# Performance work log

Measured on AMD Instinct MI355X. Metric: run time of the kernel, lower is better.

The kernel has to match this reference:

```python
import jax, jax.numpy as jnp
import numpy as np
from jax import lax

INPUT_DIM = 16
H1 = 5
H2 = 50
NUM_CLASSES = 20
B = 4096
T = 512


def _lstm(x, w_ih, w_hh, b_ih, b_hh, hidden):
    # x: [B, T, D]; PyTorch LSTM gate order i, f, g, o; returns all hidden states [B, T, H]
    xg = jnp.einsum('btd,gd->btg', x, w_ih) + (b_ih + b_hh)  # [B, T, 4H]
    xg_t = jnp.swapaxes(xg, 0, 1)  # [T, B, 4H]
    h0 = jnp.zeros((x.shape[0], hidden), x.dtype)
    c0 = jnp.zeros((x.shape[0], hidden), x.dtype)

    def step(carry, xt):
        h, c = carry
        g = xt + h @ w_hh.T  # [B, 4H]
        i, f, gg, o = jnp.split(g, 4, axis=-1)
        i = jax.nn.sigmoid(i)
        f = jax.nn.sigmoid(f)
        gg = jnp.tanh(gg)
        o = jax.nn.sigmoid(o)
        c = f * c + i * gg
        h = o * jnp.tanh(c)
        return (h, c), h

    _, hs = lax.scan(step, (h0, c0), xg_t)
    return jnp.swapaxes(hs, 0, 1)  # [B, T, H]


def setup_inputs() -> dict:
    key = jax.random.key(0)
    ks = jax.random.split(key, 12)
    s1 = 1.0 / np.sqrt(H1)
    s2 = 1.0 / np.sqrt(H2)
    u = lambda k, shape, s: jax.random.uniform(k, shape, jnp.float32, -s, s)
    return {
        'x': jax.random.normal(ks[0], (B, T, INPUT_DIM), jnp.float32),
        'w_ih1': u(ks[1], (4 * H1, INPUT_DIM), s1),
        'w_hh1': u(ks[2], (4 * H1, H1), s1),
        'b_ih1': u(ks[3], (4 * H1,), s1),
        'b_hh1': u(ks[4], (4 * H1,), s1),
        'w_ih2': u(ks[5], (4 * H2, H1), s2),
        'w_hh2': u(ks[6], (4 * H2, H2), s2),
        'b_ih2': u(ks[7], (4 * H2,), s2),
        'b_hh2': u(ks[8], (4 * H2,), s2),
        'fc_w': u(ks[9], (NUM_CLASSES, H2), s2),
        'fc_b': u(ks[10], (NUM_CLASSES,), s2),
    }


def reference(x, w_ih1, w_hh1, b_ih1, b_hh1, w_ih2, w_hh2, b_ih2, b_hh2, fc_w, fc_b):
    h1 = _lstm(x, w_ih1, w_hh1, b_ih1, b_hh1, H1)   # [B, T, 5]
    h2 = _lstm(h1, w_ih2, w_hh2, b_ih2, b_hh2, H2)  # [B, T, 50]
    feat = h2[:, -1, :]  # last timestep; dropout is identity in eval mode
    out = feat @ fc_w.T + fc_b  # [B, num_classes]
    return (out, feat)
```

## Files before the change

kernel.cpp:

```cpp
#include <hip/hip_runtime.h>
#include <stdint.h>

#define B_TOTAL 4096
#define T_STEPS 512
#define IN_DIM 16
#define H1 5
#define H2 50
#define NCLS 20
#define XFS 40

typedef __attribute__((ext_vector_type(8))) short bf16x8;
typedef __attribute__((ext_vector_type(4))) float f32x4;

#define LOG2E 1.44269504f
#define C2L   2.88539008f
#define C2L2  5.77078016f

__device__ inline float rcp1pexp2(float y){
  return __builtin_amdgcn_rcpf(1.0f + __builtin_amdgcn_exp2f(y));
}

__device__ inline unsigned pack_top(float a, float b){
  return __builtin_amdgcn_perm(__float_as_uint(a), __float_as_uint(b), 0x07060302u);
}
__device__ inline void cvt_store(unsigned short* dh, unsigned short* dl, float4 v){
  uint2 H, L;
  H.x = pack_top(v.y, v.x);
  H.y = pack_top(v.w, v.z);
  float r0 = v.x - __uint_as_float(__float_as_uint(v.x) & 0xFFFF0000u);
  float r1 = v.y - __uint_as_float(__float_as_uint(v.y) & 0xFFFF0000u);
  float r2 = v.z - __uint_as_float(__float_as_uint(v.z) & 0xFFFF0000u);
  float r3 = v.w - __uint_as_float(__float_as_uint(v.w) & 0xFFFF0000u);
  L.x = pack_top(r1, r0);
  L.y = pack_top(r3, r2);
  *(uint2*)dh = H; *(uint2*)dl = L;
}
__device__ inline void split1(float h, unsigned short& hi, unsigned short& lo){
  unsigned u = __float_as_uint(h);
  hi = (unsigned short)(u >> 16);
  float r = h - __uint_as_float(u & 0xFFFF0000u);
  lo = (unsigned short)(__float_as_uint(r) >> 16);
}
__device__ inline void wsplit(float w, short& hi, short& lo){
  unsigned u = __float_as_uint(w);
  hi = (short)(u >> 16);
  float r = w - __uint_as_float(u & 0xFFFF0000u);
  lo = (short)(__float_as_uint(r) >> 16);
}
__device__ inline void xsplit(float4 a, float4 b, bf16x8& H, bf16x8& L){
  short h,l;
  wsplit(a.x,h,l); H[0]=h; L[0]=l;
  wsplit(a.y,h,l); H[1]=h; L[1]=l;
  wsplit(a.z,h,l); H[2]=h; L[2]=l;
  wsplit(a.w,h,l); H[3]=h; L[3]=l;
  wsplit(b.x,h,l); H[4]=h; L[4]=l;
  wsplit(b.y,h,l); H[5]=h; L[5]=l;
  wsplit(b.z,h,l); H[6]=h; L[6]=l;
  wsplit(b.w,h,l); H[7]=h; L[7]=l;
}

#define LDS_FENCE() __asm__ volatile("s_waitcnt lgkmcnt(0)" ::: "memory")
#define BARRIER()   __asm__ volatile("s_barrier" ::: "memory")

__global__ __launch_bounds__(256, 1) void lstm_fused_kernel(
    const float* __restrict__ x,
    const float* __restrict__ w_ih1, const float* __restrict__ w_hh1,
    const float* __restrict__ b_ih1, const float* __restrict__ b_hh1,
    const float* __restrict__ w_ih2, const float* __restrict__ w_hh2,
    const float* __restrict__ b_ih2, const float* __restrict__ b_hh2,
    const float* __restrict__ fc_w, const float* __restrict__ fc_b,
    float* __restrict__ out)
{
  const int tid  = threadIdx.x;
  const int lane = tid & 63;
  const int wave = tid >> 6;
  const int l15  = lane & 15;
  const int quad = lane >> 4;
  const int b0   = blockIdx.x * 16;

  __shared__ __align__(16) unsigned short a2h[2][16*72], a2l[2][16*72];
  __shared__ __align__(16) unsigned short xfh[2][16*XFS], xfl[2][16*XFS];
  __shared__ float h2f[16*52];

  const bf16x8 zero8 = {0,0,0,0,0,0,0,0};
  const f32x4  zero4 = {0.f,0.f,0.f,0.f};

  bf16x8 Bh[4][3], Bl[4][3];
  f32x4 biasv[4];
  float cst[4] = {0.f,0.f,0.f,0.f};

  const int rsw = ((l15 >> 3) & 1) << 3;
  const int wsw = (quad >> 1) << 3;

#pragma unroll
  for (int tt=0; tt<4; ++tt)
#pragma unroll
    for (int kt=0; kt<3; ++kt){ Bh[tt][kt]=zero8; Bl[tt][kt]=zero8; }

  if (wave < 3){
    const int c = wave*16 + l15;
#pragma unroll
    for (int tt=0; tt<4; ++tt){
      const float gsc = (tt == 2) ? C2L : LOG2E;
      const int grow = tt*H2 + c;
#pragma unroll
      for (int kt=0; kt<2; ++kt){
#pragma unroll
        for (int j=0;j<8;j++){
          const int kk = kt*32 + quad*8 + j;
          float w = 0.f;
          if (kk < H2)         w = w_hh2[grow*H2 + kk];
          else if (kk < H2+H1) w = w_ih2[grow*H1 + (kk-H2)];
          w *= gsc;
          short hi, lo; wsplit(w, hi, lo);
          Bh[tt][kt][j] = hi; Bl[tt][kt][j] = lo;
        }
      }
      const float bias = gsc * (b_ih2[grow] + b_hh2[grow]);
      biasv[tt][0]=bias; biasv[tt][1]=bias; biasv[tt][2]=bias; biasv[tt][3]=bias;
    }
  } else {
#pragma unroll
    for (int tt=0; tt<4; ++tt){
      const float gsc = (tt == 2) ? C2L : LOG2E;
      float bias = 0.f;
      if (l15 < 2){
        const int grow = tt*H2 + 48 + l15;
#pragma unroll
        for (int kt=0; kt<2; ++kt){
#pragma unroll
          for (int j=0;j<8;j++){
            const int kk = kt*32 + quad*8 + j;
            float w = 0.f;
            if (kk < H2)         w = w_hh2[grow*H2 + kk];
            else if (kk < H2+H1) w = w_ih2[grow*H1 + (kk-H2)];
            w *= gsc;
            short hi, lo; wsplit(w, hi, lo);
            Bh[tt][kt][j] = hi; Bl[tt][kt][j] = lo;
          }
        }
        bias = gsc * (b_ih2[grow] + b_hh2[grow]);
      } else if (l15 < 7){
        const int e = l15 - 2;
        const int grow = tt*H1 + e;
#pragma unroll
        for (int j=0;j<8;j++){
          const int kk = 32 + quad*8 + j;
          float w1 = (kk >= H2 && kk < H2+H1) ? gsc * w_hh1[grow*H1 + (kk-H2)] : 0.f;
          short hi, lo; wsplit(w1, hi, lo);
          Bh[tt][1][j] = hi; Bl[tt][1][j] = lo;
          const int k2 = quad*8 + j;
          float w2 = (k2 < IN_DIM) ? gsc * w_ih1[grow*IN_DIM + k2] : 0.f;
          wsplit(w2, hi, lo);
          Bh[tt][2][j] = hi; Bl[tt][2][j] = lo;
        }
        bias = gsc * (b_ih1[grow] + b_hh1[grow]);
      }
      biasv[tt][0]=bias; biasv[tt][1]=bias; biasv[tt][2]=bias; biasv[tt][3]=bias;
    }
  }

  { unsigned short* p = &a2h[0][0]; for (int i=tid;i<2*16*72;i+=256)  p[i]=0; }
  { unsigned short* p = &a2l[0][0]; for (int i=tid;i<2*16*72;i+=256)  p[i]=0; }
  { unsigned short* p = &xfh[0][0]; for (int i=tid;i<2*16*XFS;i+=256) p[i]=0; }
  { unsigned short* p = &xfl[0][0]; for (int i=tid;i<2*16*XFS;i+=256) p[i]=0; }
  __syncthreads();

  const bool xprod = (wave == 0);
  const int pxb = lane >> 2;
  const int pxd = (lane & 3) * 4;
  const float* pxbase = &x[(size_t)(b0+pxb)*T_STEPS*IN_DIM + pxd];
  float4 PA, PB;
  if (xprod){
    float4 v1 = *(const float4*)(pxbase + 1*IN_DIM);
    cvt_store(&xfh[1][pxb*XFS+pxd], &xfl[1][pxb*XFS+pxd], v1);
    PA = *(const float4*)(pxbase + 2*IN_DIM);
  }

  if (wave == 3){
    bf16x8 XAh = zero8, XAl = zero8;
    if (quad < 2){
      const float* xp = &x[(size_t)(b0+l15)*T_STEPS*IN_DIM + quad*8];
      xsplit(*(const float4*)xp, *(const float4*)(xp+4), XAh, XAl);
    }
    f32x4 acc[4];
#pragma unroll
    for (int tt=0; tt<4; ++tt){
      f32x4 c2 = __builtin_amdgcn_mfma_f32_16x16x32_bf16(XAh, Bh[tt][2], biasv[tt], 0,0,0);
      c2 = __builtin_amdgcn_mfma_f32_16x16x32_bf16(XAl, Bh[tt][2], c2, 0,0,0);
      c2 = __builtin_amdgcn_mfma_f32_16x16x32_bf16(XAh, Bl[tt][2], c2, 0,0,0);
      acc[tt] = c2;
    }
    const bool isl1 = (l15 >= 2) && (l15 < 7);
#pragma unroll
    for (int r=0;r<4;r++){
      float gi = rcp1pexp2(-acc[0][r]);
      float gf = rcp1pexp2(-acc[1][r]);
      float gg = fmaf(-C2L2, rcp1pexp2(acc[2][r]), C2L);
      float go = rcp1pexp2(-acc[3][r]);
      float cn = fmaf(gf, cst[r], gi * gg);
      if (isl1){
        cst[r] = cn;
        float h = go * fmaf(-2.0f, rcp1pexp2(cn), 1.0f);
        unsigned short hh, hl; split1(h, hh, hl);
        const int row = quad*4 + r;
        a2h[0][row*72 + ((48 + l15) ^ wsw)] = hh;
        a2l[0][row*72 + ((48 + l15) ^ wsw)] = hl;
      }
    }
  }
  LDS_FENCE(); BARRIER();

#define MAIN_BODY(T_, RD_, WR_, PXW_, PXL_, LAST_) do { \
    if (xprod){ \
      cvt_store(&xfh[RD_][pxb*XFS+pxd], &xfl[RD_][pxb*XFS+pxd], PXW_);  \
      const int nidx_ = ((T_)+3 < T_STEPS) ? (T_)+3 : T_STEPS-1; \
      PXL_ = *(const float4*)(pxbase + (size_t)nidx_*IN_DIM);           \
    } \
    const int rb_ = l15*72; \
    bf16x8 ah0 = *(const bf16x8*)&a2h[RD_][rb_ +      ((quad*8) ^ rsw)]; \
    bf16x8 al0 = *(const bf16x8*)&a2l[RD_][rb_ +      ((quad*8) ^ rsw)]; \
    bf16x8 ah1 = *(const bf16x8*)&a2h[RD_][rb_ + 32 + ((quad*8) ^ rsw)]; \
    bf16x8 al1 = *(const bf16x8*)&a2l[RD_][rb_ + 32 + ((quad*8) ^ rsw)]; \
    f32x4 acc[4]; \
    if (wave < 3){ \
      _Pragma("unroll") \
      for (int tt=0; tt<4; ++tt){ \
        f32x4 c0 = __builtin_amdgcn_mfma_f32_16x16x32_bf16(ah0, Bh[tt][0], biasv[tt], 0,0,0); \
        c0 = __builtin_amdgcn_mfma_f32_16x16x32_bf16(al0, Bh[tt][0], c0, 0,0,0); \
        c0 = __builtin_amdgcn_mfma_f32_16x16x32_bf16(ah0, Bl[tt][0], c0, 0,0,0); \
        f32x4 c1 = __builtin_amdgcn_mfma_f32_16x16x32_bf16(ah1, Bh[tt][1], zero4, 0,0,0); \
        c1 = __builtin_amdgcn_mfma_f32_16x16x32_bf16(al1, Bh[tt][1], c1, 0,0,0); \
        c1 = __builtin_amdgcn_mfma_f32_16x16x32_bf16(ah1, Bl[tt][1], c1, 0,0,0); \
        acc[tt] = c0 + c1; \
      } \
    } else { \
      bf16x8 xfH = *(const bf16x8*)&xfh[WR_][l15*XFS + quad*8]; \
      bf16x8 xfL = *(const bf16x8*)&xfl[WR_][l15*XFS + quad*8]; \
      _Pragma("unroll") \
      for (int tt=0; tt<4; ++tt){ \
        f32x4 c0 = __builtin_amdgcn_mfma_f32_16x16x32_bf16(ah0, Bh[tt][0], biasv[tt], 0,0,0); \
        c0 = __builtin_amdgcn_mfma_f32_16x16x32_bf16(al0, Bh[tt][0], c0, 0,0,0); \
        c0 = __builtin_amdgcn_mfma_f32_16x16x32_bf16(ah0, Bl[tt][0], c0, 0,0,0); \
        f32x4 c1 = __builtin_amdgcn_mfma_f32_16x16x32_bf16(ah1, Bh[tt][1], zero4, 0,0,0); \
        c1 = __builtin_amdgcn_mfma_f32_16x16x32_bf16(al1, Bh[tt][1], c1, 0,0,0); \
        c1 = __builtin_amdgcn_mfma_f32_16x16x32_bf16(ah1, Bl[tt][1], c1, 0,0,0); \
        f32x4 c2 = __builtin_amdgcn_mfma_f32_16x16x32_bf16(xfH, Bh[tt][2], zero4, 0,0,0); \
        c2 = __builtin_amdgcn_mfma_f32_16x16x32_bf16(xfL, Bh[tt][2], c2, 0,0,0); \
        c2 = __builtin_amdgcn_mfma_f32_16x16x32_bf16(xfH, Bl[tt][2], c2, 0,0,0); \
        acc[tt] = (c0 + c1) + c2; \
      } \
    } \
     \
    if (wave < 3){ \
      const int wrb = quad*4*72 + ((wave*16 + l15) ^ wsw); \
      _Pragma("unroll") \
      for (int r=0;r<4;r++){ \
        float gi = rcp1pexp2(-acc[0][r]); \
        float gf = rcp1pexp2(-acc[1][r]); \
        float gg = fmaf(-C2L2, rcp1pexp2(acc[2][r]), C2L); \
        float go = rcp1pexp2(-acc[3][r]); \
        cst[r] = fmaf(gf, cst[r], gi * gg); \
        float h = go * fmaf(-2.0f, rcp1pexp2(cst[r]), 1.0f); \
        unsigned short hh, hl; split1(h, hh, hl); \
        a2h[WR_][wrb + r*72] = hh; \
        a2l[WR_][wrb + r*72] = hl; \
        if (LAST_){ \
          out[(size_t)B_TOTAL*NCLS + (size_t)(b0+quad*4+r)*H2 + wave*16+l15] = h; \
          h2f[(quad*4+r)*52 + wave*16+l15] = h; \
        } \
      } \
    } else { \
      const int wrb = quad*4*72 + ((48 + l15) ^ wsw);   \
      const bool wv_ = l15 < 7; \
      _Pragma("unroll") \
      for (int r=0;r<4;r++){ \
        float gi = rcp1pexp2(-acc[0][r]); \
        float gf = rcp1pexp2(-acc[1][r]); \
        float gg = fmaf(-C2L2, rcp1pexp2(acc[2][r]), C2L); \
        float go = rcp1pexp2(-acc[3][r]); \
        cst[r] = fmaf(gf, cst[r], gi * gg); \
        float h = go * fmaf(-2.0f, rcp1pexp2(cst[r]), 1.0f); \
        if (wv_){ \
          unsigned short hh, hl; split1(h, hh, hl); \
          a2h[WR_][wrb + r*72] = hh; \
          a2l[WR_][wrb + r*72] = hl; \
          if (LAST_ && l15 < 2){ \
            out[(size_t)B_TOTAL*NCLS + (size_t)(b0+quad*4+r)*H2 + 48+l15] = h; \
            h2f[(quad*4+r)*52 + 48+l15] = h; \
          } \
        } \
      } \
    } \
  } while(0)

  for (int t2 = 0; t2 < T_STEPS-2; t2 += 2){
    MAIN_BODY(t2,   0, 1, PA, PB, 0);
    LDS_FENCE(); BARRIER();
    MAIN_BODY(t2+1, 1, 0, PB, PA, 0);
    LDS_FENCE(); BARRIER();
  }
  MAIN_BODY(T_STEPS-2, 0, 1, PA, PB, 0);
  LDS_FENCE(); BARRIER();
  MAIN_BODY(T_STEPS-1, 1, 0, PB, PA, 1);

#undef MAIN_BODY

  __syncthreads();
  for (int i = tid; i < 16*NCLS; i += 256){
    const int b = i / NCLS, o = i % NCLS;
    float s = fc_b[o];
#pragma unroll 10
    for (int k=0;k<H2;k++) s += fc_w[o*H2+k] * h2f[b*52+k];
    out[(size_t)(b0+b)*NCLS + o] = s;
  }
}

extern "C" void kernel_launch(void* const* d_in, const int* in_sizes, int n_in,
                              void* d_out, int out_size, void* d_ws, size_t ws_size,
                              hipStream_t stream) {
  const float* x     = (const float*)d_in[0];
  const float* w_ih1 = (const float*)d_in[1];
  const float* w_hh1 = (const float*)d_in[2];
  const float* b_ih1 = (const float*)d_in[3];
  const float* b_hh1 = (const float*)d_in[4];
  const float* w_ih2 = (const float*)d_in[5];
  const float* w_hh2 = (const float*)d_in[6];
  const float* b_ih2 = (const float*)d_in[7];
  const float* b_hh2 = (const float*)d_in[8];
  const float* fc_w  = (const float*)d_in[9];
  const float* fc_b  = (const float*)d_in[10];
  float* out = (float*)d_out;

  lstm_fused_kernel<<<dim3(B_TOTAL/16), dim3(256), 0, stream>>>(
      x, w_ih1, w_hh1, b_ih1, b_hh1, w_ih2, w_hh2, b_ih2, b_hh2, fc_w, fc_b, out);
}
```

Measured before the change: 592.8 us.

## Process two 16-row batch groups per block to interleave independent recurrences

Each block now handles 32 batch rows as two independent 16-row groups, with separate cell state, x prefetch and LDS buffers. Both groups' MFMA chains and activations are interleaved within each timestep, so the latency of one group can overlap with work on the other. The cost is half as many blocks, which leaves half the CUs idle on a 256-CU part, and more register and LDS use per block.

```diff
diff --git a/kernel.cpp b/kernel.cpp
--- a/kernel.cpp
+++ b/kernel.cpp
@@ -76,18 +76,19 @@
   const int wave = tid >> 6;
   const int l15  = lane & 15;
   const int quad = lane >> 4;
-  const int b0   = blockIdx.x * 16;
-
-  __shared__ __align__(16) unsigned short a2h[2][16*72], a2l[2][16*72];
-  __shared__ __align__(16) unsigned short xfh[2][16*XFS], xfl[2][16*XFS];
-  __shared__ float h2f[16*52];
+  const int b0   = blockIdx.x * 32;
+
+  __shared__ __align__(16) unsigned short a2h[2][32*72], a2l[2][32*72];
+  __shared__ __align__(16) unsigned short xfh[2][32*XFS], xfl[2][32*XFS];
+  __shared__ float h2f[32*52];
 
   const bf16x8 zero8 = {0,0,0,0,0,0,0,0};
   const f32x4  zero4 = {0.f,0.f,0.f,0.f};
 
   bf16x8 Bh[4][3], Bl[4][3];
   f32x4 biasv[4];
-  float cst[4] = {0.f,0.f,0.f,0.f};
+  float cstA[4] = {0.f,0.f,0.f,0.f};
+  float cstB[4] = {0.f,0.f,0.f,0.f};
 
   const int rsw = ((l15 >> 3) & 1) << 3;
   const int wsw = (quad >> 1) << 3;
@@ -160,69 +161,113 @@
     }
   }
 
-  { unsigned short* p = &a2h[0][0]; for (int i=tid;i<2*16*72;i+=256)  p[i]=0; }
-  { unsigned short* p = &a2l[0][0]; for (int i=tid;i<2*16*72;i+=256)  p[i]=0; }
-  { unsigned short* p = &xfh[0][0]; for (int i=tid;i<2*16*XFS;i+=256) p[i]=0; }
-  { unsigned short* p = &xfl[0][0]; for (int i=tid;i<2*16*XFS;i+=256) p[i]=0; }
+  { unsigned short* p = &a2h[0][0]; for (int i=tid;i<2*32*72;i+=256)  p[i]=0; }
+  { unsigned short* p = &a2l[0][0]; for (int i=tid;i<2*32*72;i+=256)  p[i]=0; }
+  { unsigned short* p = &xfh[0][0]; for (int i=tid;i<2*32*XFS;i+=256) p[i]=0; }
+  { unsigned short* p = &xfl[0][0]; for (int i=tid;i<2*32*XFS;i+=256) p[i]=0; }
   __syncthreads();
 
   const bool xprod = (wave == 0);
   const int pxb = lane >> 2;
   const int pxd = (lane & 3) * 4;
-  const float* pxbase = &x[(size_t)(b0+pxb)*T_STEPS*IN_DIM + pxd];
-  float4 PA, PB;
+  const float* pxbaseA = &x[(size_t)(b0+pxb   )*T_STEPS*IN_DIM + pxd];
+  const float* pxbaseB = &x[(size_t)(b0+16+pxb)*T_STEPS*IN_DIM + pxd];
+  float4 PA_A, PA_B, PB_A, PB_B;
   if (xprod){
-    float4 v1 = *(const float4*)(pxbase + 1*IN_DIM);
-    cvt_store(&xfh[1][pxb*XFS+pxd], &xfl[1][pxb*XFS+pxd], v1);
-    PA = *(const float4*)(pxbase + 2*IN_DIM);
+    float4 v1a = *(const float4*)(pxbaseA + 1*IN_DIM);
+    float4 v1b = *(const float4*)(pxbaseB + 1*IN_DIM);
+    cvt_store(&xfh[1][pxb*XFS+pxd],      &xfl[1][pxb*XFS+pxd],      v1a);
+    cvt_store(&xfh[1][(16+pxb)*XFS+pxd], &xfl[1][(16+pxb)*XFS+pxd], v1b);
+    PA_A = *(const float4*)(pxbaseA + 2*IN_DIM);
+    PA_B = *(const float4*)(pxbaseB + 2*IN_DIM);
   }
 
   if (wave == 3){
-    bf16x8 XAh = zero8, XAl = zero8;
-    if (quad < 2){
-      const float* xp = &x[(size_t)(b0+l15)*T_STEPS*IN_DIM + quad*8];
-      xsplit(*(const float4*)xp, *(const float4*)(xp+4), XAh, XAl);
+#pragma unroll
+    for (int g=0; g<2; ++g){
+      bf16x8 XAh = zero8, XAl = zero8;
+      if (quad < 2){
+        const float* xp = &x[(size_t)(b0+g*16+l15)*T_STEPS*IN_DIM + quad*8];
+        xsplit(*(const float4*)xp, *(const float4*)(xp+4), XAh, XAl);
+      }
+      f32x4 acc[4];
+#pragma unroll
+      for (int tt=0; tt<4; ++tt){
+        f32x4 c2 = __builtin_amdgcn_mfma_f32_16x16x32_bf16(XAh, Bh[tt][2], biasv[tt], 0,0,0);
+        c2 = __builtin_amdgcn_mfma_f32_16x16x32_bf16(XAl, Bh[tt][2], c2, 0,0,0);
+        c2 = __builtin_amdgcn_mfma_f32_16x16x32_bf16(XAh, Bl[tt][2], c2, 0,0,0);
+        acc[tt] = c2;
+      }
+      const bool isl1 = (l15 >= 2) && (l15 < 7);
+#pragma unroll
+      for (int r=0;r<4;r++){
+        float gi = rcp1pexp2(-acc[0][r]);
+        float gf = rcp1pexp2(-acc[1][r]);
+        float gg = fmaf(-C2L2, rcp1pexp2(acc[2][r]), C2L);
+        float go = rcp1pexp2(-acc[3][r]);
+        float cn0 = (g==0) ? cstA[r] : cstB[r];
+        float cn = fmaf(gf, cn0, gi * gg);
+        if (isl1){
+          if (g==0) cstA[r] = cn; else cstB[r] = cn;
+          float h = go * fmaf(-2.0f, rcp1pexp2(cn), 1.0f);
+          unsigned short hh, hl; split1(h, hh, hl);
+          const int row = g*16 + quad*4 + r;
+          a2h[0][row*72 + ((48 + l15) ^ wsw)] = hh;
+          a2l[0][row*72 + ((48 + l15) ^ wsw)] = hl;
+        }
+      }
     }
-    f32x4 acc[4];
-#pragma unroll
-    for (int tt=0; tt<4; ++tt){
-      f32x4 c2 = __builtin_amdgcn_mfma_f32_16x16x32_bf16(XAh, Bh[tt][2], biasv[tt], 0,0,0);
-      c2 = __builtin_amdgcn_mfma_f32_16x16x32_bf16(XAl, Bh[tt][2], c2, 0,0,0);
-      c2 = __builtin_amdgcn_mfma_f32_16x16x32_bf16(XAh, Bl[tt][2], c2, 0,0,0);
-      acc[tt] = c2;
-    }
-    const bool isl1 = (l15 >= 2) && (l15 < 7);
-#pragma unroll
-    for (int r=0;r<4;r++){
-      float gi = rcp1pexp2(-acc[0][r]);
-      float gf = rcp1pexp2(-acc[1][r]);
-      float gg = fmaf(-C2L2, rcp1pexp2(acc[2][r]), C2L);
-      float go = rcp1pexp2(-acc[3][r]);
-      float cn = fmaf(gf, cst[r], gi * gg);
-      if (isl1){
-        cst[r] = cn;
-        float h = go * fmaf(-2.0f, rcp1pexp2(cn), 1.0f);
-        unsigned short hh, hl; split1(h, hh, hl);
-        const int row = quad*4 + r;
-        a2h[0][row*72 + ((48 + l15) ^ wsw)] = hh;
-        a2l[0][row*72 + ((48 + l15) ^ wsw)] = hl;
-      }
-    }
   }
   LDS_FENCE(); BARRIER();
 
-#define MAIN_BODY(T_, RD_, WR_, PXW_, PXL_, LAST_) do { \
-    if (xprod){ \
-      cvt_store(&xfh[RD_][pxb*XFS+pxd], &xfl[RD_][pxb*XFS+pxd], PXW_);  \
-      const int nidx_ = ((T_)+3 < T_STEPS) ? (T_)+3 : T_STEPS-1; \
-      PXL_ = *(const float4*)(pxbase + (size_t)nidx_*IN_DIM);           \
+#define ACT_STORE(ACC_, CST_, GO_, WR_, LAST_) do { \
+    if (wave < 3){ \
+      const int wrb = ((GO_) + quad*4)*72 + ((wave*16 + l15) ^ wsw); \
+      _Pragma("unroll") \
+      for (int r=0;r<4;r++){ \
+        float gi = rcp1pexp2(-ACC_[0][r]); \
+        float gf = rcp1pexp2(-ACC_[1][r]); \
+        float gg = fmaf(-C2L2, rcp1pexp2(ACC_[2][r]), C2L); \
+        float go = rcp1pexp2(-ACC_[3][r]); \
+        CST_[r] = fmaf(gf, CST_[r], gi * gg); \
+        float h = go * fmaf(-2.0f, rcp1pexp2(CST_[r]), 1.0f); \
+        unsigned short hh, hl; split1(h, hh, hl); \
+        a2h[WR_][wrb + r*72] = hh; \
+        a2l[WR_][wrb + r*72] = hl; \
+        if (LAST_){ \
+          out[(size_t)B_TOTAL*NCLS + (size_t)(b0+(GO_)+quad*4+r)*H2 + wave*16+l15] = h; \
+          h2f[((GO_)+quad*4+r)*52 + wave*16+l15] = h; \
+        } \
+      } \
+    } else { \
+      const int wrb = ((GO_) + quad*4)*72 + ((48 + l15) ^ wsw); \
+      const bool wv_ = l15 < 7; \
+      _Pragma("unroll") \
+      for (int r=0;r<4;r++){ \
+        float gi = rcp1pexp2(-ACC_[0][r]); \
+        float gf = rcp1pexp2(-ACC_[1][r]); \
+        float gg = fmaf(-C2L2, rcp1pexp2(ACC_[2][r]), C2L); \
+        float go = rcp1pexp2(-ACC_[3][r]); \
+        CST_[r] = fmaf(gf, CST_[r], gi * gg); \
+        float h = go * fmaf(-2.0f, rcp1pexp2(CST_[r]), 1.0f); \
+        if (wv_){ \
+          unsigned short hh, hl; split1(h, hh, hl); \
+          a2h[WR_][wrb + r*72] = hh; \
+          a2l[WR_][wrb + r*72] = hl; \
+          if ((LAST_) && l15 < 2){ \
+            out[(size_t)B_TOTAL*NCLS + (size_t)(b0+(GO_)+quad*4+r)*H2 + 48+l15] = h; \
+            h2f[((GO_)+quad*4+r)*52 + 48+l15] = h; \
+          } \
+        } \
+      } \
     } \
-    const int rb_ = l15*72; \
-    bf16x8 ah0 = *(const bf16x8*)&a2h[RD_][rb_ +      ((quad*8) ^ rsw)]; \
-    bf16x8 al0 = *(const bf16x8*)&a2l[RD_][rb_ +      ((quad*8) ^ rsw)]; \
-    bf16x8 ah1 = *(const bf16x8*)&a2h[RD_][rb_ + 32 + ((quad*8) ^ rsw)]; \
-    bf16x8 al1 = *(const bf16x8*)&a2l[RD_][rb_ + 32 + ((quad*8) ^ rsw)]; \
-    f32x4 acc[4]; \
+  } while(0)
+
+#define GROUP_MFMA(ACC_, RB_, XH_, XL_) do { \
+    bf16x8 ah0 = *(const bf16x8*)&a2h[RD__][(RB_) +      ((quad*8) ^ rsw)]; \
+    bf16x8 al0 = *(const bf16x8*)&a2l[RD__][(RB_) +      ((quad*8) ^ rsw)]; \
+    bf16x8 ah1 = *(const bf16x8*)&a2h[RD__][(RB_) + 32 + ((quad*8) ^ rsw)]; \
+    bf16x8 al1 = *(const bf16x8*)&a2l[RD__][(RB_) + 32 + ((quad*8) ^ rsw)]; \
     if (wave < 3){ \
       _Pragma("unroll") \
       for (int tt=0; tt<4; ++tt){ \
@@ -232,11 +277,9 @@
         f32x4 c1 = __builtin_amdgcn_mfma_f32_16x16x32_bf16(ah1, Bh[tt][1], zero4, 0,0,0); \
         c1 = __builtin_amdgcn_mfma_f32_16x16x32_bf16(al1, Bh[tt][1], c1, 0,0,0); \
         c1 = __builtin_amdgcn_mfma_f32_16x16x32_bf16(ah1, Bl[tt][1], c1, 0,0,0); \
-        acc[tt] = c0 + c1; \
+        ACC_[tt] = c0 + c1; \
       } \
     } else { \
-      bf16x8 xfH = *(const bf16x8*)&xfh[WR_][l15*XFS + quad*8]; \
-      bf16x8 xfL = *(const bf16x8*)&xfl[WR_][l15*XFS + quad*8]; \
       _Pragma("unroll") \
       for (int tt=0; tt<4; ++tt){ \
         f32x4 c0 = __builtin_amdgcn_mfma_f32_16x16x32_bf16(ah0, Bh[tt][0], biasv[tt], 0,0,0); \
@@ -245,69 +288,53 @@
         f32x4 c1 = __builtin_amdgcn_mfma_f32_16x16x32_bf16(ah1, Bh[tt][1], zero4, 0,0,0); \
         c1 = __builtin_amdgcn_mfma_f32_16x16x32_bf16(al1, Bh[tt][1], c1, 0,0,0); \
         c1 = __builtin_amdgcn_mfma_f32_16x16x32_bf16(ah1, Bl[tt][1], c1, 0,0,0); \
-        f32x4 c2 = __builtin_amdgcn_mfma_f32_16x16x32_bf16(xfH, Bh[tt][2], zero4, 0,0,0); \
-        c2 = __builtin_amdgcn_mfma_f32_16x16x32_bf16(xfL, Bh[tt][2], c2, 0,0,0); \
-        c2 = __builtin_amdgcn_mfma_f32_16x16x32_bf16(xfH, Bl[tt][2], c2, 0,0,0); \
-        acc[tt] = (c0 + c1) + c2; \
-      } \
-    } \
-     \
-    if (wave < 3){ \
-      const int wrb = quad*4*72 + ((wave*16 + l15) ^ wsw); \
-      _Pragma("unroll") \
-      for (int r=0;r<4;r++){ \
-        float gi = rcp1pexp2(-acc[0][r]); \
-        float gf = rcp1pexp2(-acc[1][r]); \
-        float gg = fmaf(-C2L2, rcp1pexp2(acc[2][r]), C2L); \
-        float go = rcp1pexp2(-acc[3][r]); \
-        cst[r] = fmaf(gf, cst[r], gi * gg); \
-        float h = go * fmaf(-2.0f, rcp1pexp2(cst[r]), 1.0f); \
-        unsigned short hh, hl; split1(h, hh, hl); \
-        a2h[WR_][wrb + r*72] = hh; \
-        a2l[WR_][wrb + r*72] = hl; \
-        if (LAST_){ \
-          out[(size_t)B_TOTAL*NCLS + (size_t)(b0+quad*4+r)*H2 + wave*16+l15] = h; \
-          h2f[(quad*4+r)*52 + wave*16+l15] = h; \
-        } \
-      } \
-    } else { \
-      const int wrb = quad*4*72 + ((48 + l15) ^ wsw);   \
-      const bool wv_ = l15 < 7; \
-      _Pragma("unroll") \
-      for (int r=0;r<4;r++){ \
-        float gi = rcp1pexp2(-acc[0][r]); \
-        float gf = rcp1pexp2(-acc[1][r]); \
-        float gg = fmaf(-C2L2, rcp1pexp2(acc[2][r]), C2L); \
-        float go = rcp1pexp2(-acc[3][r]); \
-        cst[r] = fmaf(gf, cst[r], gi * gg); \
-        float h = go * fmaf(-2.0f, rcp1pexp2(cst[r]), 1.0f); \
-        if (wv_){ \
-          unsigned short hh, hl; split1(h, hh, hl); \
-          a2h[WR_][wrb + r*72] = hh; \
-          a2l[WR_][wrb + r*72] = hl; \
-          if (LAST_ && l15 < 2){ \
-            out[(size_t)B_TOTAL*NCLS + (size_t)(b0+quad*4+r)*H2 + 48+l15] = h; \
-            h2f[(quad*4+r)*52 + 48+l15] = h; \
-          } \
-        } \
+        f32x4 c2 = __builtin_amdgcn_mfma_f32_16x16x32_bf16(XH_, Bh[tt][2], zero4, 0,0,0); \
+        c2 = __builtin_amdgcn_mfma_f32_16x16x32_bf16(XL_, Bh[tt][2], c2, 0,0,0); \
+        c2 = __builtin_amdgcn_mfma_f32_16x16x32_bf16(XH_, Bl[tt][2], c2, 0,0,0); \
+        ACC_[tt] = (c0 + c1) + c2; \
       } \
     } \
   } while(0)
 
+#define MAIN_BODY(T_, RD_, WR_, PWA_, PWB_, PLA_, PLB_, LAST_) do { \
+    const int RD__ = (RD_); \
+    if (xprod){ \
+      cvt_store(&xfh[RD_][pxb*XFS+pxd],      &xfl[RD_][pxb*XFS+pxd],      PWA_); \
+      cvt_store(&xfh[RD_][(16+pxb)*XFS+pxd], &xfl[RD_][(16+pxb)*XFS+pxd], PWB_); \
+      const int nidx_ = ((T_)+3 < T_STEPS) ? (T_)+3 : T_STEPS-1; \
+      PLA_ = *(const float4*)(pxbaseA + (size_t)nidx_*IN_DIM); \
+      PLB_ = *(const float4*)(pxbaseB + (size_t)nidx_*IN_DIM); \
+    } \
+    bf16x8 xfHA = zero8, xfLA = zero8, xfHB = zero8, xfLB = zero8; \
+    if (wave == 3){ \
+      xfHA = *(const bf16x8*)&xfh[WR_][l15*XFS + quad*8]; \
+      xfLA = *(const bf16x8*)&xfl[WR_][l15*XFS + quad*8]; \
+      xfHB = *(const bf16x8*)&xfh[WR_][(16+l15)*XFS + quad*8]; \
+      xfLB = *(const bf16x8*)&xfl[WR_][(16+l15)*XFS + quad*8]; \
+    } \
+    f32x4 accA[4], accB[4]; \
+    GROUP_MFMA(accA, l15*72,        xfHA, xfLA); \
+    GROUP_MFMA(accB, (16+l15)*72,   xfHB, xfLB); \
+    ACT_STORE(accA, cstA, 0,  WR_, LAST_); \
+    ACT_STORE(accB, cstB, 16, WR_, LAST_); \
+  } while(0)
+
   for (int t2 = 0; t2 < T_STEPS-2; t2 += 2){
-    MAIN_BODY(t2,   0, 1, PA, PB, 0);
+    MAIN_BODY(t2,   0, 1, PA_A, PA_B, PB_A, PB_B, 0);
     LDS_FENCE(); BARRIER();
-    MAIN_BODY(t2+1, 1, 0, PB, PA, 0);
+    MAIN_BODY(t2+1, 1, 0, PB_A, PB_B, PA_A, PA_B, 0);
     LDS_FENCE(); BARRIER();
   }
-  MAIN_BODY(T_STEPS-2, 0, 1, PA, PB, 0);
+  MAIN_BODY(T_STEPS-2, 0, 1, PA_A, PA_B, PB_A, PB_B, 0);
   LDS_FENCE(); BARRIER();
-  MAIN_BODY(T_STEPS-1, 1, 0, PB, PA, 1);
+  MAIN_BODY(T_STEPS-1, 1, 0, PB_A, PB_B, PA_A, PA_B, 1);
 
 #undef MAIN_BODY
+#undef GROUP_MFMA
+#undef ACT_STORE
 
   __syncthreads();
-  for (int i = tid; i < 16*NCLS; i += 256){
+  for (int i = tid; i < 32*NCLS; i += 256){
     const int b = i / NCLS, o = i % NCLS;
     float s = fc_b[o];
 #pragma unroll 10
@@ -332,6 +359,6 @@
   const float* fc_b  = (const float*)d_in[10];
   float* out = (float*)d_out;
 
-  lstm_fused_kernel<<<dim3(B_TOTAL/16), dim3(256), 0, stream>>>(
+  lstm_fused_kernel<<<dim3(B_TOTAL/32), dim3(256), 0, stream>>>(
       x, w_ih1, w_hh1, b_ih1, b_hh1, w_ih2, w_hh2, b_ih2, b_hh2, fc_w, fc_b, out);
 }
```

After: 1.086 ms. +83.2%, slower.
